# Kernel optimization log

Hardware: AMD Instinct MI355X
Metric: run time of the kernel (lower is better)

## Reference

```python
import jax, jax.numpy as jnp
import numpy as np

B, LF, RATE = 2, 2048, 4
DF, DS, H = 1024, 1024, 8
D2 = DF // 2            # 512: both self (d1) and cross (d2) branch dims (equal split)
POOL_H = 2048
TS = LF // RATE         # 512 slow steps


def _p(key, shape):
    return jax.random.normal(key, shape, jnp.float32) * 0.02


def setup_inputs() -> dict:
    keys = iter(jax.random.split(jax.random.key(0), 32))
    inp = {
        "x_fast": jax.random.normal(next(keys), (B, LF, DF), jnp.float32),
        "x_slow": jax.random.normal(next(keys), (B, TS, DS), jnp.float32),
    }
    for name in ("fself", "fcross", "sself", "scross"):
        inp[f"{name}_wqkv"] = _p(next(keys), (D2, 3 * D2))
        inp[f"{name}_bqkv"] = jnp.zeros((3 * D2,), jnp.float32)
        inp[f"{name}_wo"] = _p(next(keys), (D2, D2))
        inp[f"{name}_bo"] = jnp.zeros((D2,), jnp.float32)
    inp["lift_w"] = _p(next(keys), (DS, D2))
    inp["lift_b"] = jnp.zeros((D2,), jnp.float32)
    inp["pool_w1"] = _p(next(keys), (RATE * DF, POOL_H))
    inp["pool_b1"] = jnp.zeros((POOL_H,), jnp.float32)
    inp["pool_w2"] = _p(next(keys), (POOL_H, D2))
    inp["pool_b2"] = jnp.zeros((D2,), jnp.float32)
    return inp


def _mha(q_in, k_in, v_in, wqkv, bqkv, wo, bo):
    """Standard multihead attention with fused in-proj weight [d, 3d]."""
    b, tq, d = q_in.shape
    hd = d // H
    q = q_in @ wqkv[:, :d] + bqkv[:d]
    k = k_in @ wqkv[:, d:2 * d] + bqkv[d:2 * d]
    v = v_in @ wqkv[:, 2 * d:] + bqkv[2 * d:]
    q = q.reshape(b, tq, H, hd)
    k = k.reshape(b, k_in.shape[1], H, hd)
    v = v.reshape(b, v_in.shape[1], H, hd)
    scores = jnp.einsum('bqhd,bkhd->bhqk', q, k) * np.float32(1.0 / np.sqrt(hd))
    w = jax.nn.softmax(scores, axis=-1)
    o = jnp.einsum('bhqk,bkhd->bqhd', w, v).reshape(b, tq, d)
    return o @ wo + bo


def _forward(x_fast, x_slow,
             fself_wqkv, fself_bqkv, fself_wo, fself_bo,
             fcross_wqkv, fcross_bqkv, fcross_wo, fcross_bo,
             sself_wqkv, sself_bqkv, sself_wo, sself_bo,
             scross_wqkv, scross_bqkv, scross_wo, scross_bo,
             lift_w, lift_b, pool_w1, pool_b1, pool_w2, pool_b2):
    b = x_fast.shape[0]
    # ---- fast level: lift slow -> fast timescale (ffn applied before repeat)
    y = jnp.repeat(x_slow @ lift_w + lift_b, RATE, axis=1)          # [B, LF, D2]
    x1, x2 = x_fast[..., :D2], x_fast[..., D2:]
    z_fast = jnp.concatenate([
        _mha(x1, x1, x1, fself_wqkv, fself_bqkv, fself_wo, fself_bo),
        _mha(x2, y, y, fcross_wqkv, fcross_bqkv, fcross_wo, fcross_bo),
    ], axis=-1)
    # ---- slow level: causal block pooling of fast sequence
    blocks = x_fast.reshape(b, TS, RATE * DF)                        # LF == TS*RATE
    s = jax.nn.gelu(blocks @ pool_w1 + pool_b1) @ pool_w2 + pool_b2  # [B, TS, D2]
    # causal shift: prepend zero slow step, drop last (zero in pooled feature dim)
    s = jnp.concatenate([jnp.zeros((b, 1, D2), s.dtype), s[:, :-1]], axis=1)
    s1, s2 = x_slow[..., :D2], x_slow[..., D2:]
    z_slow = jnp.concatenate([
        _mha(s1, s1, s1, sself_wqkv, sself_bqkv, sself_wo, sself_bo),
        _mha(s2, s, s, scross_wqkv, scross_bqkv, scross_wo, scross_bo),
    ], axis=-1)
    return z_fast, z_slow


def reference(x_fast, x_slow,
              fself_wqkv, fself_bqkv, fself_wo, fself_bo,
              fcross_wqkv, fcross_bqkv, fcross_wo, fcross_bo,
              sself_wqkv, sself_bqkv, sself_wo, sself_bo,
              scross_wqkv, scross_bqkv, scross_wo, scross_bo,
              lift_w, lift_b, pool_w1, pool_b1, pool_w2, pool_b2):
    return _forward(x_fast, x_slow,
                    fself_wqkv, fself_bqkv, fself_wo, fself_bo,
                    fcross_wqkv, fcross_bqkv, fcross_wo, fcross_bo,
                    sself_wqkv, sself_bqkv, sself_wo, sself_bo,
                    scross_wqkv, scross_bqkv, scross_wo, scross_bo,
                    lift_w, lift_b, pool_w1, pool_b1, pool_w2, pool_b2)
```

## Files before the change

### kernel.cpp

```cpp
#include <hip/hip_runtime.h>
#include <hip/hip_bf16.h>


typedef __attribute__((ext_vector_type(8))) short bf16x8;
typedef __attribute__((ext_vector_type(4))) float f32x4;
typedef unsigned short u16;
typedef unsigned int u32;

__device__ inline u16 f2bf(float f) {
    __hip_bfloat16 h = __float2bfloat16(f);
    return *reinterpret_cast<u16*>(&h);
}
__device__ inline u32 pack2(float a, float b) {
    return (u32)f2bf(a) | ((u32)f2bf(b) << 16);
}
__device__ inline float bf2f(u16 h) {
    u32 x = ((u32)h) << 16; float f;
    __builtin_memcpy(&f, &x, 4);
    return f;
}
__device__ inline void gld16(const u16* g, u16* l) {
    __builtin_amdgcn_global_load_lds(
        (const __attribute__((address_space(1))) void*)(g),
        (__attribute__((address_space(3))) void*)(l), 16, 0, 0);
}
template <int N>
__device__ inline void wait_vmcnt() {
    if constexpr (N == 0)      asm volatile("s_waitcnt vmcnt(0)" ::: "memory");
    else if constexpr (N == 4) asm volatile("s_waitcnt vmcnt(4)" ::: "memory");
    else if constexpr (N == 8) asm volatile("s_waitcnt vmcnt(8)" ::: "memory");
}

struct GDesc {
    const u16* A; const u16* Bt; const float* bias;
    void* out0; u16* aux0; u16* aux1;
    int lda, ldb, ldc, K, ntx, mode, rshift, tile_end;
};
struct GPack { int n; int pad[3]; GDesc d[8]; };

template <int TMT>
__global__ __launch_bounds__(256)
void gemm_multi(GPack pk)
{
    constexpr int TM = TMT * 16;
    constexpr int W = TMT / 2;
    constexpr int BUF = TM * 64;
    constexpr int NLD = TM / 32 * 2;
    __shared__ u16 As[2 * BUF];
    __shared__ u16 Bs[2 * BUF];

    int bid = blockIdx.x;
    int di = 0;
    while (bid >= pk.d[di].tile_end) ++di;
    const GDesc g = pk.d[di];
    const int base = di ? pk.d[di - 1].tile_end : 0;
    const int local = bid - base;
    const int ty = local / g.ntx, tx = local - ty * g.ntx;
    const int row0 = ty * TM, col0 = tx * TM;

    const int t = threadIdx.x;
    const int wave = t >> 6, lane = t & 63;
    const int l15 = lane & 15, quad = lane >> 4;
    const int wm = (wave >> 1) * W * 16, wn = (wave & 1) * W * 16;

    const int srow = wave * 8 + (lane >> 3);
    const int ssw = (((lane & 7) ^ (lane >> 3))) * 8;
    const u16* Ag = g.A + (long long)(row0 + srow) * g.lda + ssw;
    const u16* Bg = g.Bt + (long long)(col0 + srow) * g.ldb + ssw;

    const int c0 = (quad ^ (l15 & 7)) * 8;

    f32x4 acc[W][W];
#pragma unroll
    for (int i = 0; i < W; ++i)
#pragma unroll
        for (int j = 0; j < W; ++j) {
            acc[i][j][0] = 0.f; acc[i][j][1] = 0.f;
            acc[i][j][2] = 0.f; acc[i][j][3] = 0.f;
        }

    auto stage = [&](int buf, int k0) {
#pragma unroll
        for (int r = 0; r < TM / 32; ++r) {
            gld16(Ag + (long long)r * 32 * g.lda + k0, As + buf * BUF + r * 2048 + wave * 512);
            gld16(Bg + (long long)r * 32 * g.ldb + k0, Bs + buf * BUF + r * 2048 + wave * 512);
        }
    };
    auto compute = [&](int buf) {
        const u16* Ab = As + buf * BUF;
        const u16* Bb = Bs + buf * BUF;
#pragma unroll
        for (int kc = 0; kc < 2; ++kc) {
            const int cc = kc ? (c0 ^ 32) : c0;
            bf16x8 af[W], bfr[W];
#pragma unroll
            for (int i = 0; i < W; ++i) {
                af[i]  = *(const bf16x8*)(Ab + (wm + i * 16 + l15) * 64 + cc);
                bfr[i] = *(const bf16x8*)(Bb + (wn + i * 16 + l15) * 64 + cc);
            }
#pragma unroll
            for (int i = 0; i < W; ++i)
#pragma unroll
                for (int j = 0; j < W; ++j)
                    acc[i][j] = __builtin_amdgcn_mfma_f32_16x16x32_bf16(af[i], bfr[j], acc[i][j], 0, 0, 0);
        }
    };

    const int nt = g.K >> 6;
    stage(0, 0);
    for (int tt = 0; tt < nt; ++tt) {
        const int cur = tt & 1;
        if (tt + 1 < nt) {
            stage(cur ^ 1, (tt + 1) << 6);
            wait_vmcnt<NLD>();
        } else {
            wait_vmcnt<0>();
        }
        __builtin_amdgcn_sched_barrier(0);
        __builtin_amdgcn_s_barrier();
        __builtin_amdgcn_sched_barrier(0);
        compute(cur);
        __builtin_amdgcn_sched_barrier(0);
        __builtin_amdgcn_s_barrier();
    }

    const int rmask = (1 << g.rshift) - 1;
#pragma unroll
    for (int i = 0; i < W; ++i)
#pragma unroll
        for (int j = 0; j < W; ++j)
#pragma unroll
            for (int r = 0; r < 4; ++r) {
                int m = row0 + wm + i * 16 + quad * 4 + r;
                int n = col0 + wn + j * 16 + l15;
                float v = acc[i][j][r];
                if (g.mode != 5) v += g.bias[n];
                if (g.mode == 0) {
                    ((float*)g.out0)[(long long)m * g.ldc + n] = v;
                } else if (g.mode == 1 || g.mode == 5) {
                    ((u16*)g.out0)[(long long)m * g.ldc + n] = f2bf(v);
                } else if (g.mode == 2) {
                    float x3 = v * v * v;
                    v = 0.5f * v * (1.f + tanhf(0.7978845608028654f * (v + 0.044715f * x3)));
                    ((u16*)g.out0)[(long long)m * g.ldc + n] = f2bf(v);
                } else if (g.mode == 3) {
                    u16 h = f2bf(v);
                    if (n < 512) ((u16*)g.out0)[(long long)m * 512 + n] = h;
                    else if (n < 1024) g.aux0[(long long)m * 512 + (n - 512)] = h;
                    else {
                        int d = n - 1024;
                        int bb = m >> g.rshift, rr = m & rmask;
                        g.aux1[((long long)((bb * 8 + (d >> 6)) * 64 + (d & 63)) << g.rshift) + rr] = h;
                    }
                } else if (g.mode == 4) {
                    u16 h = f2bf(v);
                    if (n < 512) ((u16*)g.out0)[(long long)m * 512 + n] = h;
                    else {
                        int d = n - 512;
                        int bb = m >> g.rshift, rr = m & rmask;
                        g.aux1[((long long)((bb * 8 + (d >> 6)) * 64 + (d & 63)) << g.rshift) + rr] = h;
                    }
                } else {
                    int t9 = m & 511;
                    if (t9 != 511) ((u16*)g.out0)[(long long)(m + 1) * g.ldc + n] = f2bf(v);
                    if (t9 == 0)  ((u16*)g.out0)[(long long)m * g.ldc + n] = 0;
                }
            }
}

#define ALD 72

struct ADesc { const u16* Q; const u16* K; const u16* Vt; u16* O; int Rq, nk, tile_end, pad; };
struct APack { int n; int pad[3]; ADesc d[4]; };

__global__ __launch_bounds__(256)
void attn_multi(APack pk, float prescale)
{
    __shared__ u16 Qs[64 * 64];
    __shared__ u16 Ks[2 * 64 * 64];
    __shared__ u16 Vts[2 * 64 * 64];
    __shared__ u16 Ps[4][16 * ALD];

    int bid = blockIdx.x;
    int di = 0;
    while (bid >= pk.d[di].tile_end) ++di;
    const ADesc g = pk.d[di];
    const int base = di ? pk.d[di - 1].tile_end : 0;
    const int local = bid - base;

    const int t = threadIdx.x;
    const int wave = t >> 6, lane = t & 63;
    const int l15 = lane & 15, quad = lane >> 4;
    const int bh = local & 15, b = bh >> 3, h = bh & 7;
    const int q0 = (local >> 4) * 64;
    const int nk = g.nk;

    const int srow = wave * 8 + (lane >> 3);
    const int ssw = (((lane & 7) ^ (lane >> 3))) * 8;
    const int c0 = (quad ^ (l15 & 7)) * 8;

    const u16* Qg = g.Q + ((long long)(b * g.Rq + q0 + srow) << 9) + h * 64 + ssw;
    const u16* Kg = g.K + ((long long)(b * nk + srow) << 9) + h * 64 + ssw;
    const u16* Vg = g.Vt + (long long)bh * 64 * nk + (long long)srow * nk + ssw;

    auto stage = [&](int buf, int kt) {
#pragma unroll
        for (int r = 0; r < 2; ++r) {
            gld16(Kg + ((long long)(kt + r * 32) << 9), Ks + buf * 4096 + r * 2048 + wave * 512);
            gld16(Vg + (long long)r * 32 * nk + kt, Vts + buf * 4096 + r * 2048 + wave * 512);
        }
    };

#pragma unroll
    for (int r = 0; r < 2; ++r)
        gld16(Qg + ((long long)r * 32 << 9), Qs + r * 2048 + wave * 512);
    stage(0, 0);
    wait_vmcnt<4>();
    __builtin_amdgcn_sched_barrier(0);
    __builtin_amdgcn_s_barrier();
    __builtin_amdgcn_sched_barrier(0);

    bf16x8 qf[2];
    qf[0] = *(const bf16x8*)(Qs + (wave * 16 + l15) * 64 + c0);
    qf[1] = *(const bf16x8*)(Qs + (wave * 16 + l15) * 64 + (c0 ^ 32));

    f32x4 Oacc[4];
#pragma unroll
    for (int nt2 = 0; nt2 < 4; ++nt2) { Oacc[nt2][0] = 0.f; Oacc[nt2][1] = 0.f; Oacc[nt2][2] = 0.f; Oacc[nt2][3] = 0.f; }
    float lr[4] = {0.f, 0.f, 0.f, 0.f};

    u16* Pw = &Ps[wave][0];

    auto acompute = [&](int buf) {
        const u16* Kb = Ks + buf * 4096;
        const u16* Vb = Vts + buf * 4096;
#pragma unroll
        for (int k16 = 0; k16 < 4; ++k16) {
            f32x4 s;
            s[0] = 0.f; s[1] = 0.f; s[2] = 0.f; s[3] = 0.f;
            bf16x8 kf0 = *(const bf16x8*)(Kb + (k16 * 16 + l15) * 64 + c0);
            bf16x8 kf1 = *(const bf16x8*)(Kb + (k16 * 16 + l15) * 64 + (c0 ^ 32));
            s = __builtin_amdgcn_mfma_f32_16x16x32_bf16(qf[0], kf0, s, 0, 0, 0);
            s = __builtin_amdgcn_mfma_f32_16x16x32_bf16(qf[1], kf1, s, 0, 0, 0);
#pragma unroll
            for (int r = 0; r < 4; ++r) {
                float p = exp2f(s[r] * prescale);
                lr[r] += p;
                Pw[(quad * 4 + r) * ALD + k16 * 16 + l15] = f2bf(p);
            }
        }
        bf16x8 pf0 = *(const bf16x8*)(Pw + l15 * ALD + quad * 8);
        bf16x8 pf1 = *(const bf16x8*)(Pw + l15 * ALD + 32 + quad * 8);
#pragma unroll
        for (int nt2 = 0; nt2 < 4; ++nt2) {
            bf16x8 vf0 = *(const bf16x8*)(Vb + (nt2 * 16 + l15) * 64 + c0);
            bf16x8 vf1 = *(const bf16x8*)(Vb + (nt2 * 16 + l15) * 64 + (c0 ^ 32));
            Oacc[nt2] = __builtin_amdgcn_mfma_f32_16x16x32_bf16(pf0, vf0, Oacc[nt2], 0, 0, 0);
            Oacc[nt2] = __builtin_amdgcn_mfma_f32_16x16x32_bf16(pf1, vf1, Oacc[nt2], 0, 0, 0);
        }
    };

    const int nt = nk >> 6;
    for (int tt = 0; tt < nt; ++tt) {
        const int cur = tt & 1;
        if (tt + 1 < nt) {
            stage(cur ^ 1, (tt + 1) << 6);
            wait_vmcnt<4>();
        } else {
            wait_vmcnt<0>();
        }
        __builtin_amdgcn_sched_barrier(0);
        __builtin_amdgcn_s_barrier();
        __builtin_amdgcn_sched_barrier(0);
        acompute(cur);
        __builtin_amdgcn_sched_barrier(0);
        __builtin_amdgcn_s_barrier();
    }

    float inv[4];
#pragma unroll
    for (int r = 0; r < 4; ++r) {
        float s = lr[r];
#pragma unroll
        for (int off = 1; off < 16; off <<= 1) s += __shfl_xor(s, off);
        inv[r] = 1.f / s;
    }

    u16* Ob = g.O + ((long long)(b * g.Rq + q0 + wave * 16 + quad * 4) << 9) + h * 64;
#pragma unroll
    for (int nt2 = 0; nt2 < 4; ++nt2)
#pragma unroll
        for (int r = 0; r < 4; ++r)
            Ob[(long long)r * 512 + nt2 * 16 + l15] = f2bf(Oacc[nt2][r] * inv[r]);
}

struct WDesc { const float* src; u16* dst; int ldn, K, tx_, tile_end; };
struct WPack { int n; int pad[3]; WDesc d[12]; };

__global__ __launch_bounds__(256)
void wt_multi(WPack pk)
{
    __shared__ float T[64][68];
    int bid = blockIdx.x;
    int di = 0;
    while (bid >= pk.d[di].tile_end) ++di;
    const WDesc g = pk.d[di];
    const int base = di ? pk.d[di - 1].tile_end : 0;
    const int local = bid - base;
    const int k0 = (local % g.tx_) * 64;
    const int n0 = (local / g.tx_) * 64;
    const int t = threadIdx.x;
#pragma unroll
    for (int i = 0; i < 4; ++i) {
        int idx = t + i * 256;
        int r = idx >> 4, c4 = idx & 15;
        float4 v = *(const float4*)(g.src + (long long)(k0 + r) * g.ldn + n0 + c4 * 4);
        T[r][c4 * 4 + 0] = v.x; T[r][c4 * 4 + 1] = v.y;
        T[r][c4 * 4 + 2] = v.z; T[r][c4 * 4 + 3] = v.w;
    }
    __syncthreads();
#pragma unroll
    for (int i = 0; i < 4; ++i) {
        int idx = t + i * 256;
        int rn = idx >> 4, k4 = idx & 15;
        uint2 u;
        u.x = pack2(T[k4 * 4 + 0][rn], T[k4 * 4 + 1][rn]);
        u.y = pack2(T[k4 * 4 + 2][rn], T[k4 * 4 + 3][rn]);
        *(uint2*)(g.dst + (long long)(n0 + rn) * g.K + k0 + k4 * 4) = u;
    }
}

__global__ __launch_bounds__(256)
void c_cvt2(const float* __restrict__ a, u16* __restrict__ da, int na8,
            const float* __restrict__ b, u16* __restrict__ db)
{
    int i = blockIdx.x * 256 + threadIdx.x;
    const float* s; u16* d;
    if (i < na8) { s = a + (long long)i * 8; d = da + (long long)i * 8; }
    else { s = b + (long long)(i - na8) * 8; d = db + (long long)(i - na8) * 8; }
    float4 x = *(const float4*)s;
    float4 y = *(const float4*)(s + 4);
    uint4 u;
    u.x = pack2(x.x, x.y); u.y = pack2(x.z, x.w);
    u.z = pack2(y.x, y.y); u.w = pack2(y.z, y.w);
    *(uint4*)d = u;
}

__global__ __launch_bounds__(256)
void gelu_sum(u16* __restrict__ p0, const u16* __restrict__ p1,
              const float* __restrict__ bias)
{
    int i8 = (blockIdx.x * 256 + threadIdx.x) * 8;
    uint4 a = *(const uint4*)(p0 + i8);
    uint4 b = *(const uint4*)(p1 + i8);
    int n = i8 & 2047;
    float4 bi0 = *(const float4*)(bias + n);
    float4 bi1 = *(const float4*)(bias + n + 4);
    float bb[8] = {bi0.x, bi0.y, bi0.z, bi0.w, bi1.x, bi1.y, bi1.z, bi1.w};
    u32 aw[4] = {a.x, a.y, a.z, a.w};
    u32 bw[4] = {b.x, b.y, b.z, b.w};
    u32 ow[4];
#pragma unroll
    for (int k = 0; k < 4; ++k) {
        float v0 = bf2f((u16)(aw[k] & 0xffff)) + bf2f((u16)(bw[k] & 0xffff)) + bb[2 * k];
        float v1 = bf2f((u16)(aw[k] >> 16)) + bf2f((u16)(bw[k] >> 16)) + bb[2 * k + 1];
        float x3 = v0 * v0 * v0;
        v0 = 0.5f * v0 * (1.f + tanhf(0.7978845608028654f * (v0 + 0.044715f * x3)));
        x3 = v1 * v1 * v1;
        v1 = 0.5f * v1 * (1.f + tanhf(0.7978845608028654f * (v1 + 0.044715f * x3)));
        ow[k] = pack2(v0, v1);
    }
    uint4 o; o.x = ow[0]; o.y = ow[1]; o.z = ow[2]; o.w = ow[3];
    *(uint4*)(p0 + i8) = o;
}

extern "C" void kernel_launch(void* const* d_in, const int* in_sizes, int n_in,
                              void* d_out, int out_size, void* d_ws, size_t ws_size,
                              hipStream_t stream)
{
    const float* x_fast      = (const float*)d_in[0];
    const float* x_slow      = (const float*)d_in[1];
    const float* fself_wqkv  = (const float*)d_in[2];
    const float* fself_bqkv  = (const float*)d_in[3];
    const float* fself_wo    = (const float*)d_in[4];
    const float* fself_bo    = (const float*)d_in[5];
    const float* fcross_wqkv = (const float*)d_in[6];
    const float* fcross_bqkv = (const float*)d_in[7];
    const float* fcross_wo   = (const float*)d_in[8];
    const float* fcross_bo   = (const float*)d_in[9];
    const float* sself_wqkv  = (const float*)d_in[10];
    const float* sself_bqkv  = (const float*)d_in[11];
    const float* sself_wo    = (const float*)d_in[12];
    const float* sself_bo    = (const float*)d_in[13];
    const float* scross_wqkv = (const float*)d_in[14];
    const float* scross_bqkv = (const float*)d_in[15];
    const float* scross_wo   = (const float*)d_in[16];
    const float* scross_bo   = (const float*)d_in[17];
    const float* lift_w      = (const float*)d_in[18];
    const float* lift_b      = (const float*)d_in[19];
    const float* pool_w1     = (const float*)d_in[20];
    const float* pool_b1     = (const float*)d_in[21];
    const float* pool_w2     = (const float*)d_in[22];
    const float* pool_b2     = (const float*)d_in[23];

    float* out = (float*)d_out;
    float* zf = out;
    float* zs = out + 2LL * 2048 * 1024;

    float* ws = (float*)d_ws;
    u16* pw1T     = (u16*)(ws + 0);
    u16* wqkvT_f  = (u16*)(ws + 4194304);
    u16* wqkvT_c  = (u16*)(ws + 4587520);
    u16* wqkvT_s  = (u16*)(ws + 4980736);
    u16* wqkvT_sc = (u16*)(ws + 5373952);
    u16* liftT    = (u16*)(ws + 5767168);
    u16* pw2T     = (u16*)(ws + 6029312);
    u16* woT_f    = (u16*)(ws + 6553600);
    u16* woT_c    = (u16*)(ws + 6684672);
    u16* woT_s    = (u16*)(ws + 6815744);
    u16* woT_sc   = (u16*)(ws + 6946816);
    u16* xfb      = (u16*)(ws + 7077888);
    u16* xsb      = (u16*)(ws + 9175040);
    u16* q1       = (u16*)(ws + 9699328);
    u16* k1       = (u16*)(ws + 10747904);
    u16* vt1      = (u16*)(ws + 11796480);
    u16* qs       = (u16*)(ws + 12845056);
    u16* ks       = (u16*)(ws + 13107200);
    u16* vts      = (u16*)(ws + 13369344);
    u16* qcs      = (u16*)(ws + 13631488);
    u16* k2    = (u16*)(ws + 0);
    u16* vt2   = (u16*)(ws + 262144);
    u16* sbufS = (u16*)(ws + 524288);
    u16* kcs   = (u16*)(ws + 786432);
    u16* vtcs  = (u16*)(ws + 1048576);
    u16* fo1   = (u16*)(ws + 1310720);
    u16* fo2   = (u16*)(ws + 2359296);
    u16* so1   = (u16*)(ws + 3407872);
    u16* so2   = (u16*)(ws + 3670016);
    u16* q2   = (u16*)(out + 0);
    u16* ybuf = (u16*)(out + 1048576);
    u16* hbuf = (u16*)(out + 1310720);
    u16* p1b  = (u16*)(out + 2359296);

    hipLaunchKernelGGL(c_cvt2, dim3(2560), dim3(256), 0, stream,
                       x_fast, xfb, 524288, x_slow, xsb);

    {
        WPack p; p.n = 11;
        int te = 0, i = 0;
        auto add = [&](const float* s, u16* d, int ldn, int K, int N) {
            te += (K / 64) * (N / 64);
            p.d[i++] = WDesc{s, d, ldn, K, K / 64, te};
        };
        add(pool_w1, pw1T, 2048, 4096, 2048);
        add(fself_wqkv, wqkvT_f, 1536, 512, 1536);
        add(fcross_wqkv, wqkvT_c, 1536, 512, 1536);
        add(sself_wqkv, wqkvT_s, 1536, 512, 1536);
        add(scross_wqkv, wqkvT_sc, 1536, 512, 1536);
        add(lift_w, liftT, 512, 1024, 512);
        add(pool_w2, pw2T, 512, 2048, 512);
        add(fself_wo, woT_f, 512, 512, 512);
        add(fcross_wo, woT_c, 512, 512, 512);
        add(sself_wo, woT_s, 512, 512, 512);
        add(scross_wo, woT_sc, 512, 512, 512);
        hipLaunchKernelGGL(wt_multi, dim3(te), dim3(256), 0, stream, p);
    }

    auto gl = [&](GPack& p, int i, const u16* A, int lda,
                  const u16* Bt, int ldb, const float* bias,
                  void* out0, int ldc, int M, int N, int K, int mode,
                  u16* aux0, u16* aux1, int rshift, int TM, int& te) {
        te += (M / TM) * (N / TM);
        p.d[i] = GDesc{A, Bt, bias, out0, aux0, aux1,
                       lda, ldb, ldc, K, N / TM, mode, rshift, te};
    };

    {
        GPack p; p.n = 7; int te = 0;
        gl(p, 0, xfb, 4096, pw1T, 4096, pool_b1, hbuf, 2048,
           1024, 2048, 2048, 5, 0, 0, 0, 128, te);
        gl(p, 1, xfb + 2048, 4096, pw1T + 2048, 4096, pool_b1, p1b, 2048,
           1024, 2048, 2048, 5, 0, 0, 0, 128, te);
        gl(p, 2, xfb, 1024, wqkvT_f, 512, fself_bqkv, q1, 512,
           4096, 1536, 512, 3, k1, vt1, 11, 128, te);
        gl(p, 3, xfb + 512, 1024, wqkvT_c, 512, fcross_bqkv, q2, 512,
           4096, 512, 512, 1, 0, 0, 0, 128, te);
        gl(p, 4, xsb, 1024, wqkvT_s, 512, sself_bqkv, qs, 512,
           1024, 1536, 512, 3, ks, vts, 9, 128, te);
        gl(p, 5, xsb, 1024, liftT, 1024, lift_b, ybuf, 512,
           1024, 512, 1024, 1, 0, 0, 0, 128, te);
        gl(p, 6, xsb + 512, 1024, wqkvT_sc, 512, scross_bqkv, qcs, 512,
           1024, 512, 512, 1, 0, 0, 0, 128, te);
        hipLaunchKernelGGL(gemm_multi<8>, dim3(te), dim3(256), 0, stream, p);
    }

    hipLaunchKernelGGL(gelu_sum, dim3(1024), dim3(256), 0, stream, hbuf, p1b, pool_b1);

    {
        GPack p; p.n = 2; int te = 0;
        gl(p, 0, ybuf, 512, wqkvT_c + 512 * 512, 512, fcross_bqkv + 512, k2, 512,
           1024, 1024, 512, 4, 0, vt2, 9, 64, te);
        gl(p, 1, hbuf, 2048, pw2T, 2048, pool_b2, sbufS, 512,
           1024, 512, 2048, 6, 0, 0, 0, 64, te);
        hipLaunchKernelGGL(gemm_multi<4>, dim3(te), dim3(256), 0, stream, p);
    }

    {
        GPack p; p.n = 1; int te = 0;
        gl(p, 0, sbufS, 512, wqkvT_sc + 512 * 512, 512, scross_bqkv + 512, kcs, 512,
           1024, 1024, 512, 4, 0, vtcs, 9, 64, te);
        hipLaunchKernelGGL(gemm_multi<4>, dim3(te), dim3(256), 0, stream, p);
    }

    {
        APack p; p.n = 4;
        int te = 0, i = 0;
        auto add = [&](const u16* Q, const u16* K, const u16* Vt, u16* O, int Rq, int nk) {
            te += (Rq / 64) * 16;
            p.d[i++] = ADesc{Q, K, Vt, O, Rq, nk, te, 0};
        };
        add(q1, k1, vt1, fo1, 2048, 2048);
        add(q2, k2, vt2, fo2, 2048, 512);
        add(qs, ks, vts, so1, 512, 512);
        add(qcs, kcs, vtcs, so2, 512, 512);
        hipLaunchKernelGGL(attn_multi, dim3(te), dim3(256), 0, stream, p,
                           0.125f * 1.4426950408889634f);
    }

    {
        GPack p; p.n = 4; int te = 0;
        gl(p, 0, fo1, 512, woT_f, 512, fself_bo, zf, 1024,
           4096, 512, 512, 0, 0, 0, 0, 128, te);
        gl(p, 1, fo2, 512, woT_c, 512, fcross_bo, zf + 512, 1024,
           4096, 512, 512, 0, 0, 0, 0, 128, te);
        gl(p, 2, so1, 512, woT_s, 512, sself_bo, zs, 1024,
           1024, 512, 512, 0, 0, 0, 0, 128, te);
        gl(p, 3, so2, 512, woT_sc, 512, scross_bo, zs + 512, 1024,
           1024, 512, 512, 0, 0, 0, 0, 128, te);
        hipLaunchKernelGGL(gemm_multi<8>, dim3(te), dim3(256), 0, stream, p);
    }
}
```

Baseline: 359.9 us.

## Merge all stages into one fat kernel and overlap independent work across launches

After: 368.8 us. 1.02x slower.

```diff
diff --git a/kernel.cpp b/kernel.cpp
--- a/kernel.cpp
+++ b/kernel.cpp
@@ -38,18 +38,25 @@
 };
 struct GPack { int n; int pad[3]; GDesc d[8]; };
 
+struct ADesc { const u16* Q; const u16* K; const u16* Vt; u16* O; int Rq, nk, tile_end, q0b; };
+struct APack { int n; int pad[3]; ADesc d[2]; };
+
+struct WDesc { const float* src; u16* dst; int ldn, K, tx_, tile_end; };
+struct WPack { int n; int pad[3]; WDesc d[6]; };
+
+struct CvtA { const float* a; u16* da; int na8; const float* b; u16* db; };
+struct GeluA { u16* p0; const u16* p1; const float* bias; };
+
 template <int TMT>
-__global__ __launch_bounds__(256)
-void gemm_multi(GPack pk)
+__device__ __forceinline__ void gemm_body(const GPack& pk, int bid, u16* smem)
 {
     constexpr int TM = TMT * 16;
     constexpr int W = TMT / 2;
     constexpr int BUF = TM * 64;
     constexpr int NLD = TM / 32 * 2;
-    __shared__ u16 As[2 * BUF];
-    __shared__ u16 Bs[2 * BUF];
-
-    int bid = blockIdx.x;
+    u16* As = smem;
+    u16* Bs = smem + 2 * BUF;
+
     int di = 0;
     while (bid >= pk.d[di].tile_end) ++di;
     const GDesc g = pk.d[di];
@@ -98,11 +105,13 @@
                 af[i]  = *(const bf16x8*)(Ab + (wm + i * 16 + l15) * 64 + cc);
                 bfr[i] = *(const bf16x8*)(Bb + (wn + i * 16 + l15) * 64 + cc);
             }
+            __builtin_amdgcn_s_setprio(1);
 #pragma unroll
             for (int i = 0; i < W; ++i)
 #pragma unroll
                 for (int j = 0; j < W; ++j)
                     acc[i][j] = __builtin_amdgcn_mfma_f32_16x16x32_bf16(af[i], bfr[j], acc[i][j], 0, 0, 0);
+            __builtin_amdgcn_s_setprio(0);
         }
     };
 
@@ -170,18 +179,13 @@
 
 #define ALD 72
 
-struct ADesc { const u16* Q; const u16* K; const u16* Vt; u16* O; int Rq, nk, tile_end, pad; };
-struct APack { int n; int pad[3]; ADesc d[4]; };
-
-__global__ __launch_bounds__(256)
-void attn_multi(APack pk, float prescale)
-{
-    __shared__ u16 Qs[64 * 64];
-    __shared__ u16 Ks[2 * 64 * 64];
-    __shared__ u16 Vts[2 * 64 * 64];
-    __shared__ u16 Ps[4][16 * ALD];
-
-    int bid = blockIdx.x;
+__device__ __forceinline__ void attn_body(const APack& pk, int bid, u16* smem, float prescale)
+{
+    u16* Qs  = smem;
+    u16* Ks  = smem + 4096;
+    u16* Vts = smem + 12288;
+    u16* Psb = smem + 20480;
+
     int di = 0;
     while (bid >= pk.d[di].tile_end) ++di;
     const ADesc g = pk.d[di];
@@ -192,7 +196,7 @@
     const int wave = t >> 6, lane = t & 63;
     const int l15 = lane & 15, quad = lane >> 4;
     const int bh = local & 15, b = bh >> 3, h = bh & 7;
-    const int q0 = (local >> 4) * 64;
+    const int q0 = g.q0b + (local >> 4) * 64;
     const int nk = g.nk;
 
     const int srow = wave * 8 + (lane >> 3);
@@ -229,7 +233,7 @@
     for (int nt2 = 0; nt2 < 4; ++nt2) { Oacc[nt2][0] = 0.f; Oacc[nt2][1] = 0.f; Oacc[nt2][2] = 0.f; Oacc[nt2][3] = 0.f; }
     float lr[4] = {0.f, 0.f, 0.f, 0.f};
 
-    u16* Pw = &Ps[wave][0];
+    u16* Pw = Psb + wave * 16 * ALD;
 
     auto acompute = [&](int buf) {
         const u16* Kb = Ks + buf * 4096;
@@ -240,8 +244,10 @@
             s[0] = 0.f; s[1] = 0.f; s[2] = 0.f; s[3] = 0.f;
             bf16x8 kf0 = *(const bf16x8*)(Kb + (k16 * 16 + l15) * 64 + c0);
             bf16x8 kf1 = *(const bf16x8*)(Kb + (k16 * 16 + l15) * 64 + (c0 ^ 32));
+            __builtin_amdgcn_s_setprio(1);
             s = __builtin_amdgcn_mfma_f32_16x16x32_bf16(qf[0], kf0, s, 0, 0, 0);
             s = __builtin_amdgcn_mfma_f32_16x16x32_bf16(qf[1], kf1, s, 0, 0, 0);
+            __builtin_amdgcn_s_setprio(0);
 #pragma unroll
             for (int r = 0; r < 4; ++r) {
                 float p = exp2f(s[r] * prescale);
@@ -251,6 +257,7 @@
         }
         bf16x8 pf0 = *(const bf16x8*)(Pw + l15 * ALD + quad * 8);
         bf16x8 pf1 = *(const bf16x8*)(Pw + l15 * ALD + 32 + quad * 8);
+        __builtin_amdgcn_s_setprio(1);
 #pragma unroll
         for (int nt2 = 0; nt2 < 4; ++nt2) {
             bf16x8 vf0 = *(const bf16x8*)(Vb + (nt2 * 16 + l15) * 64 + c0);
@@ -258,6 +265,7 @@
             Oacc[nt2] = __builtin_amdgcn_mfma_f32_16x16x32_bf16(pf0, vf0, Oacc[nt2], 0, 0, 0);
             Oacc[nt2] = __builtin_amdgcn_mfma_f32_16x16x32_bf16(pf1, vf1, Oacc[nt2], 0, 0, 0);
         }
+        __builtin_amdgcn_s_setprio(0);
     };
 
     const int nt = nk >> 6;
@@ -294,14 +302,9 @@
             Ob[(long long)r * 512 + nt2 * 16 + l15] = f2bf(Oacc[nt2][r] * inv[r]);
 }
 
-struct WDesc { const float* src; u16* dst; int ldn, K, tx_, tile_end; };
-struct WPack { int n; int pad[3]; WDesc d[12]; };
-
-__global__ __launch_bounds__(256)
-void wt_multi(WPack pk)
-{
-    __shared__ float T[64][68];
-    int bid = blockIdx.x;
+__device__ __forceinline__ void wt_body(const WPack& pk, int bid, u16* smem)
+{
+    float* T = (float*)smem;
     int di = 0;
     while (bid >= pk.d[di].tile_end) ++di;
     const WDesc g = pk.d[di];
@@ -315,8 +318,8 @@
         int idx = t + i * 256;
         int r = idx >> 4, c4 = idx & 15;
         float4 v = *(const float4*)(g.src + (long long)(k0 + r) * g.ldn + n0 + c4 * 4);
-        T[r][c4 * 4 + 0] = v.x; T[r][c4 * 4 + 1] = v.y;
-        T[r][c4 * 4 + 2] = v.z; T[r][c4 * 4 + 3] = v.w;
+        T[r * 68 + c4 * 4 + 0] = v.x; T[r * 68 + c4 * 4 + 1] = v.y;
+        T[r * 68 + c4 * 4 + 2] = v.z; T[r * 68 + c4 * 4 + 3] = v.w;
     }
     __syncthreads();
 #pragma unroll
@@ -324,20 +327,18 @@
         int idx = t + i * 256;
         int rn = idx >> 4, k4 = idx & 15;
         uint2 u;
-        u.x = pack2(T[k4 * 4 + 0][rn], T[k4 * 4 + 1][rn]);
-        u.y = pack2(T[k4 * 4 + 2][rn], T[k4 * 4 + 3][rn]);
+        u.x = pack2(T[(k4 * 4 + 0) * 68 + rn], T[(k4 * 4 + 1) * 68 + rn]);
+        u.y = pack2(T[(k4 * 4 + 2) * 68 + rn], T[(k4 * 4 + 3) * 68 + rn]);
         *(uint2*)(g.dst + (long long)(n0 + rn) * g.K + k0 + k4 * 4) = u;
     }
 }
 
-__global__ __launch_bounds__(256)
-void c_cvt2(const float* __restrict__ a, u16* __restrict__ da, int na8,
-            const float* __restrict__ b, u16* __restrict__ db)
-{
-    int i = blockIdx.x * 256 + threadIdx.x;
+__device__ __forceinline__ void cvt_body(const CvtA& cv, int bid)
+{
+    int i = bid * 256 + threadIdx.x;
     const float* s; u16* d;
-    if (i < na8) { s = a + (long long)i * 8; d = da + (long long)i * 8; }
-    else { s = b + (long long)(i - na8) * 8; d = db + (long long)(i - na8) * 8; }
+    if (i < cv.na8) { s = cv.a + (long long)i * 8; d = cv.da + (long long)i * 8; }
+    else { s = cv.b + (long long)(i - cv.na8) * 8; d = cv.db + (long long)(i - cv.na8) * 8; }
     float4 x = *(const float4*)s;
     float4 y = *(const float4*)(s + 4);
     uint4 u;
@@ -346,16 +347,14 @@
     *(uint4*)d = u;
 }
 
-__global__ __launch_bounds__(256)
-void gelu_sum(u16* __restrict__ p0, const u16* __restrict__ p1,
-              const float* __restrict__ bias)
-{
-    int i8 = (blockIdx.x * 256 + threadIdx.x) * 8;
-    uint4 a = *(const uint4*)(p0 + i8);
-    uint4 b = *(const uint4*)(p1 + i8);
+__device__ __forceinline__ void gelu_body(const GeluA& ge, int bid)
+{
+    int i8 = (bid * 256 + threadIdx.x) * 8;
+    uint4 a = *(const uint4*)(ge.p0 + i8);
+    uint4 b = *(const uint4*)(ge.p1 + i8);
     int n = i8 & 2047;
-    float4 bi0 = *(const float4*)(bias + n);
-    float4 bi1 = *(const float4*)(bias + n + 4);
+    float4 bi0 = *(const float4*)(ge.bias + n);
+    float4 bi1 = *(const float4*)(ge.bias + n + 4);
     float bb[8] = {bi0.x, bi0.y, bi0.z, bi0.w, bi1.x, bi1.y, bi1.z, bi1.w};
     u32 aw[4] = {a.x, a.y, a.z, a.w};
     u32 bw[4] = {b.x, b.y, b.z, b.w};
@@ -371,7 +370,26 @@
         ow[k] = pack2(v0, v1);
     }
     uint4 o; o.x = ow[0]; o.y = ow[1]; o.z = ow[2]; o.w = ow[3];
-    *(uint4*)(p0 + i8) = o;
+    *(uint4*)(ge.p0 + i8) = o;
+}
+
+template <int TMT>
+__global__ __launch_bounds__(256)
+void fat_multi(APack ap, GPack gp, WPack wp, GeluA ge, CvtA cv,
+               int na, int ngm, int nwt, int ncv, float prescale)
+{
+    constexpr int GB = 2 * 2 * (TMT * 16 * 64) * 2;
+    constexpr int SB = (GB > 50176) ? GB : 50176;
+    __shared__ __align__(16) u16 smem[SB / 2];
+    int bid = blockIdx.x;
+    if (bid < na) { attn_body(ap, bid, smem, prescale); return; }
+    bid -= na;
+    if (bid < ngm) { gemm_body<TMT>(gp, bid, smem); return; }
+    bid -= ngm;
+    if (bid < nwt) { wt_body(wp, bid, smem); return; }
+    bid -= nwt;
+    if (bid < ncv) { cvt_body(cv, bid); return; }
+    gelu_body(ge, bid - ncv);
 }
 
 extern "C" void kernel_launch(void* const* d_in, const int* in_sizes, int n_in,
@@ -442,29 +460,8 @@
     u16* hbuf = (u16*)(out + 1310720);
     u16* p1b  = (u16*)(out + 2359296);
 
-    hipLaunchKernelGGL(c_cvt2, dim3(2560), dim3(256), 0, stream,
-                       x_fast, xfb, 524288, x_slow, xsb);
-
-    {
-        WPack p; p.n = 11;
-        int te = 0, i = 0;
-        auto add = [&](const float* s, u16* d, int ldn, int K, int N) {
-            te += (K / 64) * (N / 64);
-            p.d[i++] = WDesc{s, d, ldn, K, K / 64, te};
-        };
-        add(pool_w1, pw1T, 2048, 4096, 2048);
-        add(fself_wqkv, wqkvT_f, 1536, 512, 1536);
-        add(fcross_wqkv, wqkvT_c, 1536, 512, 1536);
-        add(sself_wqkv, wqkvT_s, 1536, 512, 1536);
-        add(scross_wqkv, wqkvT_sc, 1536, 512, 1536);
-        add(lift_w, liftT, 512, 1024, 512);
-        add(pool_w2, pw2T, 512, 2048, 512);
-        add(fself_wo, woT_f, 512, 512, 512);
-        add(fcross_wo, woT_c, 512, 512, 512);
-        add(sself_wo, woT_s, 512, 512, 512);
-        add(scross_wo, woT_sc, 512, 512, 512);
-        hipLaunchKernelGGL(wt_multi, dim3(te), dim3(256), 0, stream, p);
-    }
+    const float PRESCALE = 0.125f * 1.4426950408889634f;
+    APack a_null{}; GPack g_null{}; WPack w_null{}; GeluA ge_null{}; CvtA cv_null{};
 
     auto gl = [&](GPack& p, int i, const u16* A, int lda,
                   const u16* Bt, int ldb, const float* bias,
@@ -474,6 +471,23 @@
         p.d[i] = GDesc{A, Bt, bias, out0, aux0, aux1,
                        lda, ldb, ldc, K, N / TM, mode, rshift, te};
     };
+
+    {
+        WPack wp; wp.n = 6; int te = 0, i = 0;
+        auto add = [&](const float* s, u16* d, int ldn, int K, int N) {
+            te += (K / 64) * (N / 64);
+            wp.d[i++] = WDesc{s, d, ldn, K, K / 64, te};
+        };
+        add(pool_w1, pw1T, 2048, 4096, 2048);
+        add(fself_wqkv, wqkvT_f, 1536, 512, 1536);
+        add(fcross_wqkv, wqkvT_c, 1536, 512, 1536);
+        add(sself_wqkv, wqkvT_s, 1536, 512, 1536);
+        add(scross_wqkv, wqkvT_sc, 1536, 512, 1536);
+        add(lift_w, liftT, 512, 1024, 512);
+        CvtA cv{x_fast, xfb, 524288, x_slow, xsb};
+        hipLaunchKernelGGL(fat_multi<4>, dim3(te + 2560), dim3(256), 0, stream,
+                           a_null, g_null, wp, ge_null, cv, 0, 0, te, 2560, PRESCALE);
+    }
 
     {
         GPack p; p.n = 7; int te = 0;
@@ -491,52 +505,70 @@
            1024, 512, 1024, 1, 0, 0, 0, 128, te);
         gl(p, 6, xsb + 512, 1024, wqkvT_sc, 512, scross_bqkv, qcs, 512,
            1024, 512, 512, 1, 0, 0, 0, 128, te);
-        hipLaunchKernelGGL(gemm_multi<8>, dim3(te), dim3(256), 0, stream, p);
-    }
-
-    hipLaunchKernelGGL(gelu_sum, dim3(1024), dim3(256), 0, stream, hbuf, p1b, pool_b1);
-
-    {
+        WPack wp; wp.n = 5; int wte = 0, wi = 0;
+        auto add = [&](const float* s, u16* d, int ldn, int K, int N) {
+            wte += (K / 64) * (N / 64);
+            wp.d[wi++] = WDesc{s, d, ldn, K, K / 64, wte};
+        };
+        add(pool_w2, pw2T, 512, 2048, 512);
+        add(fself_wo, woT_f, 512, 512, 512);
+        add(fcross_wo, woT_c, 512, 512, 512);
+        add(sself_wo, woT_s, 512, 512, 512);
+        add(scross_wo, woT_sc, 512, 512, 512);
+        hipLaunchKernelGGL(fat_multi<8>, dim3(te + wte), dim3(256), 0, stream,
+                           a_null, p, wp, ge_null, cv_null, 0, te, wte, 0, PRESCALE);
+    }
+
+    {
+        APack ap; ap.n = 2;
+        ap.d[0] = ADesc{q1, k1, vt1, fo1, 2048, 2048, 256, 0};
+        ap.d[1] = ADesc{qs, ks, vts, so1, 512, 512, 384, 0};
+        GeluA ge{hbuf, p1b, pool_b1};
+        hipLaunchKernelGGL(fat_multi<4>, dim3(384 + 1024), dim3(256), 0, stream,
+                           ap, g_null, w_null, ge, cv_null, 384, 0, 0, 0, PRESCALE);
+    }
+
+    {
+        APack ap; ap.n = 1;
+        ap.d[0] = ADesc{q1, k1, vt1, fo1, 2048, 2048, 256, 1024};
         GPack p; p.n = 2; int te = 0;
         gl(p, 0, ybuf, 512, wqkvT_c + 512 * 512, 512, fcross_bqkv + 512, k2, 512,
            1024, 1024, 512, 4, 0, vt2, 9, 64, te);
         gl(p, 1, hbuf, 2048, pw2T, 2048, pool_b2, sbufS, 512,
            1024, 512, 2048, 6, 0, 0, 0, 64, te);
-        hipLaunchKernelGGL(gemm_multi<4>, dim3(te), dim3(256), 0, stream, p);
-    }
-
-    {
+        hipLaunchKernelGGL(fat_multi<4>, dim3(256 + te), dim3(256), 0, stream,
+                           ap, p, w_null, ge_null, cv_null, 256, te, 0, 0, PRESCALE);
+    }
+
+    {
+        APack ap; ap.n = 1;
+        ap.d[0] = ADesc{q2, k2, vt2, fo2, 2048, 512, 512, 0};
         GPack p; p.n = 1; int te = 0;
         gl(p, 0, sbufS, 512, wqkvT_sc + 512 * 512, 512, scross_bqkv + 512, kcs, 512,
            1024, 1024, 512, 4, 0, vtcs, 9, 64, te);
-        hipLaunchKernelGGL(gemm_multi<4>, dim3(te), dim3(256), 0, stream, p);
-    }
-
-    {
-        APack p; p.n = 4;
-        int te = 0, i = 0;
-        auto add = [&](const u16* Q, const u16* K, const u16* Vt, u16* O, int Rq, int nk) {
-            te += (Rq / 64) * 16;
-            p.d[i++] = ADesc{Q, K, Vt, O, Rq, nk, te, 0};
-        };
-        add(q1, k1, vt1, fo1, 2048, 2048);
-        add(q2, k2, vt2, fo2, 2048, 512);
-        add(qs, ks, vts, so1, 512, 512);
-        add(qcs, kcs, vtcs, so2, 512, 512);
-        hipLaunchKernelGGL(attn_multi, dim3(te), dim3(256), 0, stream, p,
-                           0.125f * 1.4426950408889634f);
-    }
-
-    {
-        GPack p; p.n = 4; int te = 0;
+        hipLaunchKernelGGL(fat_multi<4>, dim3(512 + te), dim3(256), 0, stream,
+                           ap, p, w_null, ge_null, cv_null, 512, te, 0, 0, PRESCALE);
+    }
+
+    {
+        APack ap; ap.n = 1;
+        ap.d[0] = ADesc{qcs, kcs, vtcs, so2, 512, 512, 128, 0};
+        GPack p; p.n = 3; int te = 0;
         gl(p, 0, fo1, 512, woT_f, 512, fself_bo, zf, 1024,
-           4096, 512, 512, 0, 0, 0, 0, 128, te);
+           4096, 512, 512, 0, 0, 0, 0, 64, te);
         gl(p, 1, fo2, 512, woT_c, 512, fcross_bo, zf + 512, 1024,
-           4096, 512, 512, 0, 0, 0, 0, 128, te);
+           4096, 512, 512, 0, 0, 0, 0, 64, te);
         gl(p, 2, so1, 512, woT_s, 512, sself_bo, zs, 1024,
-           1024, 512, 512, 0, 0, 0, 0, 128, te);
-        gl(p, 3, so2, 512, woT_sc, 512, scross_bo, zs + 512, 1024,
-           1024, 512, 512, 0, 0, 0, 0, 128, te);
-        hipLaunchKernelGGL(gemm_multi<8>, dim3(te), dim3(256), 0, stream, p);
-    }
-}
+           1024, 512, 512, 0, 0, 0, 0, 64, te);
+        hipLaunchKernelGGL(fat_multi<4>, dim3(128 + te), dim3(256), 0, stream,
+                           ap, p, w_null, ge_null, cv_null, 128, te, 0, 0, PRESCALE);
+    }
+
+    {
+        GPack p; p.n = 1; int te = 0;
+        gl(p, 0, so2, 512, woT_sc, 512, scross_bo, zs + 512, 1024,
+           1024, 512, 512, 0, 0, 0, 0, 64, te);
+        hipLaunchKernelGGL(fat_multi<4>, dim3(te), dim3(256), 0, stream,
+                           a_null, p, w_null, ge_null, cv_null, 0, te, 0, 0, PRESCALE);
+    }
+}
```
